# Kernel optimization log

Measured on AMD Instinct MI355X. Metric: run time of the kernel, lower is better.

The kernel has to match this reference:

```python
import jax, jax.numpy as jnp
import numpy as np
from jax import lax

B = 32768

def setup_inputs() -> dict:
    key = jax.random.key(0)
    ks = jax.random.split(key, 8)
    return {
        "x": jax.random.normal(ks[0], (B, 784), dtype=jnp.float32),
        "w_conv": jax.random.normal(ks[1], (3, 3), dtype=jnp.float32),
        "W1": jax.random.normal(ks[2], (676, 100), dtype=jnp.float32) * 0.05,
        "b1": jax.random.normal(ks[3], (100,), dtype=jnp.float32) * 0.05,
        "W2": jax.random.normal(ks[4], (100, 100), dtype=jnp.float32) * 0.05,
        "b2": jax.random.normal(ks[5], (100,), dtype=jnp.float32) * 0.05,
        "W3": jax.random.normal(ks[6], (100, 10), dtype=jnp.float32) * 0.05,
        "b3": jax.random.normal(ks[7], (10,), dtype=jnp.float32) * 0.05,
    }


def reference(x, w_conv, W1, b1, W2, b2, W3, b3):
    # x: [B, 784] -> [B, 1, 28, 28]; valid 3x3 cross-correlation (tensordot == correlation)
    xr = x.reshape(-1, 1, 28, 28)
    k = w_conv.reshape(1, 1, 3, 3)  # [out_c, in_c, kh, kw]
    conv = lax.conv_general_dilated(
        xr, k, window_strides=(1, 1), padding="VALID",
        dimension_numbers=("NCHW", "OIHW", "NCHW"))  # [B, 1, 26, 26]
    h = conv.reshape(conv.shape[0], 26 * 26)  # [B, 676]
    h = jax.nn.relu(h @ W1 + b1)
    h = jax.nn.relu(h @ W2 + b2)
    return h @ W3 + b3  # [B, 10]
```

## Files before the change

### kernel.cpp

```cpp
#include <hip/hip_runtime.h>


typedef __attribute__((ext_vector_type(8))) short bf16x8;
typedef __attribute__((ext_vector_type(4))) float f32x4;

#define KP1 832
#define NP  112
#define K2P 128
#define BM  64
#define NT  256

#define W2T_OFF (NP * KP1)
#define W3T_OFF (W2T_OFF + NP * K2P)
#define WS_USHORTS (W3T_OFF + 16 * K2P)

__device__ __forceinline__ unsigned short f2bf(float f) {
    unsigned int u = __float_as_uint(f);
    u += 0x7FFFu + ((u >> 16) & 1u);
    return (unsigned short)(u >> 16);
}

__device__ __forceinline__ unsigned int pkbf(float a, float b) {
    unsigned int r;
    asm("v_cvt_pk_bf16_f32 %0, %1, %2" : "=v"(r) : "v"(a), "v"(b));
    return r;
}

__device__ __forceinline__ bf16x8 cvt8(float4 a, float4 b) {
    union { unsigned int w[4]; bf16x8 v; } u;
    u.w[0] = pkbf(a.x, a.y);
    u.w[1] = pkbf(a.z, a.w);
    u.w[2] = pkbf(b.x, b.y);
    u.w[3] = pkbf(b.z, b.w);
    return u.v;
}

__device__ __forceinline__ void gload_lds16(const void* g, void* l) {
    __builtin_amdgcn_global_load_lds(
        (const __attribute__((address_space(1))) unsigned int*)g,
        (__attribute__((address_space(3))) unsigned int*)l, 16, 0, 0);
}

__global__ void build_weights(const float* __restrict__ w_conv,
                              const float* __restrict__ W1,
                              const float* __restrict__ W2,
                              const float* __restrict__ W3,
                              unsigned short* __restrict__ ws) {
    const int idx = blockIdx.x * 256 + threadIdx.x;
    if (idx >= WS_USHORTS) return;
    float v = 0.f;
    if (idx < W2T_OFF) {
        const int col = idx / KP1, p = idx % KP1;
        if (col < 100 && p < 784) {
            const int y = p / 28, xx = p % 28;
#pragma unroll
            for (int ky = 0; ky < 3; ++ky) {
                const int py = y - ky;
                if (py < 0 || py >= 26) continue;
#pragma unroll
                for (int kx = 0; kx < 3; ++kx) {
                    const int px = xx - kx;
                    if (px < 0 || px >= 26) continue;
                    v += w_conv[ky * 3 + kx] * W1[(py * 26 + px) * 100 + col];
                }
            }
        }
    } else if (idx < W3T_OFF) {
        const int r = idx - W2T_OFF;
        const int col = r / K2P, k = r % K2P;
        if (col < 100 && k < 100) v = W2[k * 100 + col];
    } else {
        const int r = idx - W3T_OFF;
        const int col = r / K2P, k = r % K2P;
        if (col < 10 && k < 100) v = W3[k * 10 + col];
    }
    ws[idx] = f2bf(v);
}

__global__ __launch_bounds__(NT, 2)
void fused(const float* __restrict__ x,
           const unsigned short* __restrict__ wst,
           const float* __restrict__ b1,
           const float* __restrict__ b2,
           const float* __restrict__ b3,
           float* __restrict__ out) {
    __shared__ __attribute__((aligned(16))) float          xs[2][64][64];
    __shared__ __attribute__((aligned(16))) unsigned short bs[2][112][64];
    __shared__ __attribute__((aligned(16))) unsigned short h1[64][136];
    unsigned short (*h2)[136] = reinterpret_cast<unsigned short(*)[136]>(&xs[0][0][0]);

    const int tid  = threadIdx.x;
    const int lane = tid & 63;
    const int wv   = tid >> 6;
    const int l15  = lane & 15;
    const int lk   = lane >> 4;
    const int b0   = blockIdx.x * BM;
    const int wr   = wv * 16;

    const unsigned short* weff = wst;
    const unsigned short* w2t  = wst + W2T_OFF;
    const unsigned short* w3t  = wst + W3T_OFF;

    for (int f = lane; f < 16 * 14; f += 64) {
        const int r = wr + f / 14, c = 100 + (f % 14) * 2;
        *reinterpret_cast<unsigned int*>(&h1[r][c]) = 0u;
    }

    f32x4 acc[7];
#pragma unroll
    for (int n = 0; n < 7; ++n) acc[n] = (f32x4){0.f, 0.f, 0.f, 0.f};

    auto issue = [&](int kt, int buf) {
#pragma unroll
        for (int q = 0; q < 4; ++q) {
            const int row = wr + q * 4 + (lane >> 4);
            const int col = ((lane & 15) ^ (row & 7)) * 4;
            const float* g = x + (size_t)(b0 + row) * 784 + kt * 64 + col;
            gload_lds16(g, (void*)&xs[buf][wr + q * 4][0]);
        }
#pragma unroll
        for (int i = 0; i < 4; ++i) {
            const int j = wv + 4 * i;
            if (j < 14) {
                const int row = j * 8 + (lane >> 3);
                const int col = ((lane & 7) ^ (lane >> 3)) * 8;
                const unsigned short* g = weff + (size_t)row * KP1 + kt * 64 + col;
                gload_lds16(g, (void*)&bs[buf][j * 8][0]);
            }
        }
    };

    auto computeStage = [&](int buf) {
        const int arow = wr + l15;
        const int sA = (arow & 7) << 4;
        const int sB = (l15 & 7) << 4;
        const char* ap = (const char*)&xs[buf][arow][0];
#pragma unroll
        for (int ks = 0; ks < 2; ++ks) {
            const float4 lo = *reinterpret_cast<const float4*>(ap + ((ks * 128 + lk * 32 +  0) ^ sA));
            const float4 hi = *reinterpret_cast<const float4*>(ap + ((ks * 128 + lk * 32 + 16) ^ sA));
            const bf16x8 af = cvt8(lo, hi);
#pragma unroll
            for (int n = 0; n < 7; ++n) {
                const char* bp = (const char*)&bs[buf][n * 16 + l15][0];
                const bf16x8 bfr = *reinterpret_cast<const bf16x8*>(bp + ((ks * 64 + lk * 16) ^ sB));
                acc[n] = __builtin_amdgcn_mfma_f32_16x16x32_bf16(af, bfr, acc[n], 0, 0, 0);
            }
        }
    };

    issue(0, 0);
    __syncthreads();
#pragma unroll 1
    for (int t = 0; t < 12; ++t) {
        if (t < 11) issue(t + 1, (t + 1) & 1);
        __builtin_amdgcn_sched_barrier(0);
        computeStage(t & 1);
        __syncthreads();
    }

    {
        float4 t0 = (float4){0.f, 0.f, 0.f, 0.f}, t1 = t0;
        if (lk < 2) {
            const float* xp = x + (size_t)(b0 + wr + l15) * 784 + 768 + lk * 8;
            t0 = *reinterpret_cast<const float4*>(xp);
            t1 = *reinterpret_cast<const float4*>(xp + 4);
        }
        const bf16x8 aft = cvt8(t0, t1);
#pragma unroll
        for (int n = 0; n < 7; ++n) {
            const bf16x8 bft = *reinterpret_cast<const bf16x8*>(
                weff + (size_t)(n * 16 + l15) * KP1 + 768 + lk * 8);
            acc[n] = __builtin_amdgcn_mfma_f32_16x16x32_bf16(aft, bft, acc[n], 0, 0, 0);
        }
    }

    float bias[7];
#pragma unroll
    for (int n = 0; n < 7; ++n) {
        const int c = n * 16 + l15;
        bias[n] = (c < 100) ? b1[c] : 0.f;
    }
#pragma unroll
    for (int n = 0; n < 7; ++n) {
        const int col = n * 16 + l15;
        if (col < 100)
#pragma unroll
            for (int q = 0; q < 4; ++q) {
                const float v = fmaxf(acc[n][q] + bias[n], 0.f);
                h1[wr + lk * 4 + q][col] = f2bf(v);
            }
    }
    for (int f = lane; f < 16 * 14; f += 64) {
        const int r = wr + f / 14, c = 100 + (f % 14) * 2;
        *reinterpret_cast<unsigned int*>(&h2[r][c]) = 0u;
    }
    __builtin_amdgcn_sched_barrier(0);

    f32x4 acc2[7];
#pragma unroll
    for (int n = 0; n < 7; ++n) acc2[n] = (f32x4){0.f, 0.f, 0.f, 0.f};
#pragma unroll
    for (int ks = 0; ks < 4; ++ks) {
        const int kb = ks * 32 + lk * 8;
        const bf16x8 af = *reinterpret_cast<const bf16x8*>(&h1[wr + l15][kb]);
#pragma unroll
        for (int n = 0; n < 7; ++n) {
            const bf16x8 bfr = *reinterpret_cast<const bf16x8*>(
                w2t + (size_t)(n * 16 + l15) * K2P + kb);
            acc2[n] = __builtin_amdgcn_mfma_f32_16x16x32_bf16(af, bfr, acc2[n], 0, 0, 0);
        }
    }

#pragma unroll
    for (int n = 0; n < 7; ++n) {
        const int c = n * 16 + l15;
        bias[n] = (c < 100) ? b2[c] : 0.f;
    }
#pragma unroll
    for (int n = 0; n < 7; ++n) {
        const int col = n * 16 + l15;
        if (col < 100)
#pragma unroll
            for (int q = 0; q < 4; ++q) {
                const float v = fmaxf(acc2[n][q] + bias[n], 0.f);
                h2[wr + lk * 4 + q][col] = f2bf(v);
            }
    }
    __builtin_amdgcn_sched_barrier(0);

    f32x4 acc3 = (f32x4){0.f, 0.f, 0.f, 0.f};
#pragma unroll
    for (int ks = 0; ks < 4; ++ks) {
        const int kb = ks * 32 + lk * 8;
        const bf16x8 bfr = *reinterpret_cast<const bf16x8*>(
            w3t + (size_t)l15 * K2P + kb);
        const bf16x8 af = *reinterpret_cast<const bf16x8*>(&h2[wr + l15][kb]);
        acc3 = __builtin_amdgcn_mfma_f32_16x16x32_bf16(af, bfr, acc3, 0, 0, 0);
    }

    if (l15 < 10) {
        const float bb = b3[l15];
#pragma unroll
        for (int q = 0; q < 4; ++q) {
            const int row = b0 + wr + lk * 4 + q;
            out[(size_t)row * 10 + l15] = acc3[q] + bb;
        }
    }
}

extern "C" void kernel_launch(void* const* d_in, const int* in_sizes, int n_in,
                              void* d_out, int out_size, void* d_ws, size_t ws_size,
                              hipStream_t stream) {
    const float* x      = (const float*)d_in[0];
    const float* w_conv = (const float*)d_in[1];
    const float* W1     = (const float*)d_in[2];
    const float* b1     = (const float*)d_in[3];
    const float* W2     = (const float*)d_in[4];
    const float* b2     = (const float*)d_in[5];
    const float* W3     = (const float*)d_in[6];
    const float* b3     = (const float*)d_in[7];
    float* out = (float*)d_out;
    unsigned short* ws = (unsigned short*)d_ws;

    build_weights<<<(WS_USHORTS + 255) / 256, 256, 0, stream>>>(w_conv, W1, W2, W3, ws);
    fused<<<32768 / BM, NT, 0, stream>>>(x, ws, b1, b2, b3, out);
}
```

Before: 38.35 us.

## Switch first GEMM to triple-buffered 32-wide K tiles with vmcnt waits

The first-layer GEMM loop moves from double-buffered 64-wide K tiles to triple-buffered 32-wide tiles. Waits now use explicit s_waitcnt vmcnt(4) plus a raw barrier, so two loads stay in flight while the current stage computes. The weight buffer is padded to 128 rows so each wave loads a uniform share. The aim is more overlap of global-to-LDS loads with MFMA work. In exchange there are twice as many barriers, and the hand-set vmcnt counts must match the number of outstanding loads exactly.

```diff
diff --git a/kernel.cpp b/kernel.cpp
--- a/kernel.cpp
+++ b/kernel.cpp
@@ -6,13 +6,18 @@
 
 #define KP1 832
 #define NP  112
+#define NPB 128
 #define K2P 128
 #define BM  64
 #define NT  256
 
-#define W2T_OFF (NP * KP1)
+#define W2T_OFF (NPB * KP1)
 #define W3T_OFF (W2T_OFF + NP * K2P)
 #define WS_USHORTS (W3T_OFF + 16 * K2P)
+
+#define WAITV4 asm volatile("s_waitcnt vmcnt(4)" ::: "memory")
+#define WAITV0 asm volatile("s_waitcnt vmcnt(0)" ::: "memory")
+#define BAR    __builtin_amdgcn_s_barrier()
 
 __device__ __forceinline__ unsigned short f2bf(float f) {
     unsigned int u = __float_as_uint(f);
@@ -84,8 +89,8 @@
            const float* __restrict__ b2,
            const float* __restrict__ b3,
            float* __restrict__ out) {
-    __shared__ __attribute__((aligned(16))) float          xs[2][64][64];
-    __shared__ __attribute__((aligned(16))) unsigned short bs[2][112][64];
+    __shared__ __attribute__((aligned(16))) float          xs[3][64][32];
+    __shared__ __attribute__((aligned(16))) unsigned short bs[3][128][32];
     __shared__ __attribute__((aligned(16))) unsigned short h1[64][136];
     unsigned short (*h2)[136] = reinterpret_cast<unsigned short(*)[136]>(&xs[0][0][0]);
 
@@ -110,54 +115,59 @@
 #pragma unroll
     for (int n = 0; n < 7; ++n) acc[n] = (f32x4){0.f, 0.f, 0.f, 0.f};
 
-    auto issue = [&](int kt, int buf) {
-#pragma unroll
-        for (int q = 0; q < 4; ++q) {
-            const int row = wr + q * 4 + (lane >> 4);
-            const int col = ((lane & 15) ^ (row & 7)) * 4;
-            const float* g = x + (size_t)(b0 + row) * 784 + kt * 64 + col;
-            gload_lds16(g, (void*)&xs[buf][wr + q * 4][0]);
-        }
-#pragma unroll
-        for (int i = 0; i < 4; ++i) {
-            const int j = wv + 4 * i;
-            if (j < 14) {
-                const int row = j * 8 + (lane >> 3);
-                const int col = ((lane & 7) ^ (lane >> 3)) * 8;
-                const unsigned short* g = weff + (size_t)row * KP1 + kt * 64 + col;
-                gload_lds16(g, (void*)&bs[buf][j * 8][0]);
-            }
+    const int xrow_l = lane >> 3;
+    const int xcol_b = (((lane & 7) ^ xrow_l) * 16);
+    const int brow_l = lane >> 2;
+    const int bcol_b = (((lane & 3) ^ (brow_l & 3)) * 16);
+
+    auto issue = [&](int kt, float* xb, unsigned short* bb) {
+#pragma unroll
+        for (int q = 0; q < 2; ++q) {
+            const int r = wr + 8 * q + xrow_l;
+            const char* g = (const char*)(x + (size_t)(b0 + r) * 784 + kt * 32) + xcol_b;
+            gload_lds16(g, (void*)(xb + (size_t)(wr + 8 * q) * 32));
+        }
+#pragma unroll
+        for (int q = 0; q < 2; ++q) {
+            const int r = wv * 32 + 16 * q + brow_l;
+            const char* g = (const char*)(weff + (size_t)r * KP1 + kt * 32) + bcol_b;
+            gload_lds16(g, (void*)(bb + (size_t)(wv * 32 + 16 * q) * 32));
         }
     };
 
-    auto computeStage = [&](int buf) {
-        const int arow = wr + l15;
-        const int sA = (arow & 7) << 4;
-        const int sB = (l15 & 7) << 4;
-        const char* ap = (const char*)&xs[buf][arow][0];
-#pragma unroll
-        for (int ks = 0; ks < 2; ++ks) {
-            const float4 lo = *reinterpret_cast<const float4*>(ap + ((ks * 128 + lk * 32 +  0) ^ sA));
-            const float4 hi = *reinterpret_cast<const float4*>(ap + ((ks * 128 + lk * 32 + 16) ^ sA));
-            const bf16x8 af = cvt8(lo, hi);
-#pragma unroll
-            for (int n = 0; n < 7; ++n) {
-                const char* bp = (const char*)&bs[buf][n * 16 + l15][0];
-                const bf16x8 bfr = *reinterpret_cast<const bf16x8*>(bp + ((ks * 64 + lk * 16) ^ sB));
-                acc[n] = __builtin_amdgcn_mfma_f32_16x16x32_bf16(af, bfr, acc[n], 0, 0, 0);
-            }
+    auto computeStage = [&](const float* xb, const unsigned short* bb) {
+        const int r = wr + l15;
+        const char* ap = (const char*)(xb + (size_t)r * 32);
+        const int sA = (r & 7) << 4;
+        const float4 lo = *reinterpret_cast<const float4*>(ap + ((lk * 32) ^ sA));
+        const float4 hi = *reinterpret_cast<const float4*>(ap + ((lk * 32 + 16) ^ sA));
+        const bf16x8 af = cvt8(lo, hi);
+#pragma unroll
+        for (int n = 0; n < 7; ++n) {
+            const int rn = n * 16 + l15;
+            const char* bp = (const char*)(bb + (size_t)rn * 32);
+            const bf16x8 bfr = *reinterpret_cast<const bf16x8*>(bp + ((lk * 16) ^ ((rn & 3) << 4)));
+            acc[n] = __builtin_amdgcn_mfma_f32_16x16x32_bf16(af, bfr, acc[n], 0, 0, 0);
         }
     };
 
-    issue(0, 0);
-    __syncthreads();
+    float* X0 = &xs[0][0][0]; unsigned short* B0 = &bs[0][0][0];
+    float* X1 = &xs[1][0][0]; unsigned short* B1 = &bs[1][0][0];
+    float* X2 = &xs[2][0][0]; unsigned short* B2 = &bs[2][0][0];
+
+    issue(0, X0, B0);
+    issue(1, X1, B1);
+    WAITV4; BAR;
 #pragma unroll 1
-    for (int t = 0; t < 12; ++t) {
-        if (t < 11) issue(t + 1, (t + 1) & 1);
-        __builtin_amdgcn_sched_barrier(0);
-        computeStage(t & 1);
-        __syncthreads();
-    }
+    for (int tt = 0; tt < 7; ++tt) {
+        const int t = tt * 3;
+        issue(t + 2, X2, B2); computeStage(X0, B0); WAITV4; BAR;
+        issue(t + 3, X0, B0); computeStage(X1, B1); WAITV4; BAR;
+        issue(t + 4, X1, B1); computeStage(X2, B2); WAITV4; BAR;
+    }
+    issue(23, X2, B2); computeStage(X0, B0); WAITV4; BAR;
+    computeStage(X1, B1); WAITV0; BAR;
+    computeStage(X2, B2);
 
     {
         float4 t0 = (float4){0.f, 0.f, 0.f, 0.f}, t1 = t0;
@@ -174,6 +184,7 @@
             acc[n] = __builtin_amdgcn_mfma_f32_16x16x32_bf16(aft, bft, acc[n], 0, 0, 0);
         }
     }
+    __syncthreads();
 
     float bias[7];
 #pragma unroll
```

Measured after the change: 40.13 us. 1.05x slower.

## Triple-buffer x tiles with vmcnt waits, alias h1/h2 into x buffers, vectorize weight build

Applied to the files above, without the earlier changes.

The fused kernel now keeps three x staging buffers and prefetches x two k-steps ahead. Instead of a full __syncthreads it waits with explicit s_waitcnt vmcnt counts plus s_barrier, and the main loop is fully unrolled. h1 and h2 are placed inside the x staging area, so the extra buffer adds less LDS than it would otherwise. The weight-build kernel now computes four output columns per thread using float4 loads of W1. The aim is to hide global load latency more deeply, at the cost of depending on hand-counted vmcnt values being correct.

```diff
diff --git a/kernel.cpp b/kernel.cpp
--- a/kernel.cpp
+++ b/kernel.cpp
@@ -13,6 +13,11 @@
 #define W2T_OFF (NP * KP1)
 #define W3T_OFF (W2T_OFF + NP * K2P)
 #define WS_USHORTS (W3T_OFF + 16 * K2P)
+
+#define WAITV4 asm volatile("s_waitcnt vmcnt(4)" ::: "memory")
+#define WAITV0 asm volatile("s_waitcnt vmcnt(0)" ::: "memory")
+#define BAR    __builtin_amdgcn_s_barrier()
+#define SBAR0  __builtin_amdgcn_sched_barrier(0)
 
 __device__ __forceinline__ unsigned short f2bf(float f) {
     unsigned int u = __float_as_uint(f);
@@ -47,11 +52,12 @@
                               const float* __restrict__ W3,
                               unsigned short* __restrict__ ws) {
     const int idx = blockIdx.x * 256 + threadIdx.x;
-    if (idx >= WS_USHORTS) return;
-    float v = 0.f;
-    if (idx < W2T_OFF) {
-        const int col = idx / KP1, p = idx % KP1;
-        if (col < 100 && p < 784) {
+    const int WEFF_T = 28 * KP1;
+    if (idx < WEFF_T) {
+        const int j4 = idx / KP1, p = idx % KP1;
+        const int j = j4 * 4;
+        float a0 = 0.f, a1 = 0.f, a2 = 0.f, a3 = 0.f;
+        if (p < 784 && j4 < 25) {
             const int y = p / 28, xx = p % 28;
 #pragma unroll
             for (int ky = 0; ky < 3; ++ky) {
@@ -61,20 +67,29 @@
                 for (int kx = 0; kx < 3; ++kx) {
                     const int px = xx - kx;
                     if (px < 0 || px >= 26) continue;
-                    v += w_conv[ky * 3 + kx] * W1[(py * 26 + px) * 100 + col];
+                    const float wc = w_conv[ky * 3 + kx];
+                    const float4 w = *reinterpret_cast<const float4*>(
+                        W1 + (size_t)(py * 26 + px) * 100 + j);
+                    a0 = fmaf(wc, w.x, a0); a1 = fmaf(wc, w.y, a1);
+                    a2 = fmaf(wc, w.z, a2); a3 = fmaf(wc, w.w, a3);
                 }
             }
         }
-    } else if (idx < W3T_OFF) {
-        const int r = idx - W2T_OFF;
+        ws[(size_t)(j + 0) * KP1 + p] = f2bf(a0);
+        ws[(size_t)(j + 1) * KP1 + p] = f2bf(a1);
+        ws[(size_t)(j + 2) * KP1 + p] = f2bf(a2);
+        ws[(size_t)(j + 3) * KP1 + p] = f2bf(a3);
+    } else if (idx < WEFF_T + NP * K2P) {
+        const int r = idx - WEFF_T;
         const int col = r / K2P, k = r % K2P;
-        if (col < 100 && k < 100) v = W2[k * 100 + col];
-    } else {
-        const int r = idx - W3T_OFF;
+        float v = (col < 100 && k < 100) ? W2[k * 100 + col] : 0.f;
+        ws[W2T_OFF + r] = f2bf(v);
+    } else if (idx < WEFF_T + NP * K2P + 16 * K2P) {
+        const int r = idx - WEFF_T - NP * K2P;
         const int col = r / K2P, k = r % K2P;
-        if (col < 10 && k < 100) v = W3[k * 10 + col];
-    }
-    ws[idx] = f2bf(v);
+        float v = (col < 10 && k < 100) ? W3[k * 10 + col] : 0.f;
+        ws[W3T_OFF + r] = f2bf(v);
+    }
 }
 
 __global__ __launch_bounds__(NT, 2)
@@ -84,10 +99,11 @@
            const float* __restrict__ b2,
            const float* __restrict__ b3,
            float* __restrict__ out) {
-    __shared__ __attribute__((aligned(16))) float          xs[2][64][64];
+    __shared__ __attribute__((aligned(16))) float          xs[3][64][64];
     __shared__ __attribute__((aligned(16))) unsigned short bs[2][112][64];
-    __shared__ __attribute__((aligned(16))) unsigned short h1[64][136];
-    unsigned short (*h2)[136] = reinterpret_cast<unsigned short(*)[136]>(&xs[0][0][0]);
+    unsigned short (*h1)[136] = reinterpret_cast<unsigned short(*)[136]>(&xs[0][0][0]);
+    unsigned short (*h2)[136] = reinterpret_cast<unsigned short(*)[136]>(
+        (char*)&xs[0][0][0] + 17408);
 
     const int tid  = threadIdx.x;
     const int lane = tid & 63;
@@ -101,62 +117,70 @@
     const unsigned short* w2t  = wst + W2T_OFF;
     const unsigned short* w3t  = wst + W3T_OFF;
 
-    for (int f = lane; f < 16 * 14; f += 64) {
-        const int r = wr + f / 14, c = 100 + (f % 14) * 2;
-        *reinterpret_cast<unsigned int*>(&h1[r][c]) = 0u;
-    }
-
     f32x4 acc[7];
 #pragma unroll
     for (int n = 0; n < 7; ++n) acc[n] = (f32x4){0.f, 0.f, 0.f, 0.f};
 
-    auto issue = [&](int kt, int buf) {
+    auto issueX = [&](int kt, float* xb) {
 #pragma unroll
         for (int q = 0; q < 4; ++q) {
-            const int row = wr + q * 4 + (lane >> 4);
-            const int col = ((lane & 15) ^ (row & 7)) * 4;
-            const float* g = x + (size_t)(b0 + row) * 784 + kt * 64 + col;
-            gload_lds16(g, (void*)&xs[buf][wr + q * 4][0]);
-        }
-#pragma unroll
-        for (int i = 0; i < 4; ++i) {
-            const int j = wv + 4 * i;
-            if (j < 14) {
-                const int row = j * 8 + (lane >> 3);
-                const int col = ((lane & 7) ^ (lane >> 3)) * 8;
-                const unsigned short* g = weff + (size_t)row * KP1 + kt * 64 + col;
-                gload_lds16(g, (void*)&bs[buf][j * 8][0]);
-            }
+            const int rowbase = wr + 4 * q;
+            const int r = rowbase + (lane >> 4);
+            const int chunk = (lane & 15) ^ (r & 7);
+            const char* g = (const char*)(x + (size_t)(b0 + r) * 784 + kt * 64)
+                          + chunk * 16;
+            gload_lds16(g, (char*)xb + rowbase * 256);
         }
     };
-
-    auto computeStage = [&](int buf) {
-        const int arow = wr + l15;
-        const int sA = (arow & 7) << 4;
-        const int sB = (l15 & 7) << 4;
-        const char* ap = (const char*)&xs[buf][arow][0];
+    auto issueB = [&](int kt, unsigned short* bb) {
+#pragma unroll
+        for (int k = 0; k < 4; ++k) {
+            const int i = wv + 4 * k;
+            if (i < 14) {
+                const int rowbase = 8 * i;
+                const int r = rowbase + (lane >> 3);
+                const int chunk = (lane & 7) ^ (r & 7);
+                const char* g = (const char*)(weff + (size_t)r * KP1 + kt * 64)
+                              + chunk * 16;
+                gload_lds16(g, (char*)bb + rowbase * 128);
+            }
+        }
+    };
+
+    auto computeStage = [&](const float* xb, const unsigned short* bb) {
+        const int r = wr + l15;
+        const int sA = (r & 7) << 4;
+        const char* ap = (const char*)xb + r * 256;
 #pragma unroll
         for (int ks = 0; ks < 2; ++ks) {
-            const float4 lo = *reinterpret_cast<const float4*>(ap + ((ks * 128 + lk * 32 +  0) ^ sA));
-            const float4 hi = *reinterpret_cast<const float4*>(ap + ((ks * 128 + lk * 32 + 16) ^ sA));
+            const int base = ks * 128 + lk * 32;
+            const float4 lo = *reinterpret_cast<const float4*>(ap + ((base     ) ^ sA));
+            const float4 hi = *reinterpret_cast<const float4*>(ap + ((base + 16) ^ sA));
             const bf16x8 af = cvt8(lo, hi);
 #pragma unroll
             for (int n = 0; n < 7; ++n) {
-                const char* bp = (const char*)&bs[buf][n * 16 + l15][0];
-                const bf16x8 bfr = *reinterpret_cast<const bf16x8*>(bp + ((ks * 64 + lk * 16) ^ sB));
+                const int rn = n * 16 + l15;
+                const char* bp = (const char*)bb + rn * 128;
+                const bf16x8 bfr = *reinterpret_cast<const bf16x8*>(
+                    bp + ((ks * 64 + lk * 16) ^ ((rn & 7) << 4)));
                 acc[n] = __builtin_amdgcn_mfma_f32_16x16x32_bf16(af, bfr, acc[n], 0, 0, 0);
             }
         }
     };
 
-    issue(0, 0);
-    __syncthreads();
-#pragma unroll 1
+    float*          X[3] = {&xs[0][0][0], &xs[1][0][0], &xs[2][0][0]};
+    unsigned short* Bf[2] = {&bs[0][0][0], &bs[1][0][0]};
+
+    issueX(0, X[0]); issueB(0, Bf[0]); issueX(1, X[1]);
+    WAITV4; BAR;
+#pragma unroll
     for (int t = 0; t < 12; ++t) {
-        if (t < 11) issue(t + 1, (t + 1) & 1);
-        __builtin_amdgcn_sched_barrier(0);
-        computeStage(t & 1);
-        __syncthreads();
+        if (t < 11) issueB(t + 1, Bf[(t + 1) & 1]);
+        if (t < 10) issueX(t + 2, X[(t + 2) % 3]);
+        SBAR0;
+        computeStage(X[t % 3], Bf[t & 1]);
+        if (t < 10)      { WAITV4; BAR; }
+        else if (t == 10){ WAITV0; BAR; }
     }
 
     {
@@ -174,6 +198,7 @@
             acc[n] = __builtin_amdgcn_mfma_f32_16x16x32_bf16(aft, bft, acc[n], 0, 0, 0);
         }
     }
+    __syncthreads();
 
     float bias[7];
 #pragma unroll
@@ -193,9 +218,10 @@
     }
     for (int f = lane; f < 16 * 14; f += 64) {
         const int r = wr + f / 14, c = 100 + (f % 14) * 2;
+        *reinterpret_cast<unsigned int*>(&h1[r][c]) = 0u;
         *reinterpret_cast<unsigned int*>(&h2[r][c]) = 0u;
     }
-    __builtin_amdgcn_sched_barrier(0);
+    SBAR0;
 
     f32x4 acc2[7];
 #pragma unroll
@@ -227,7 +253,7 @@
                 h2[wr + lk * 4 + q][col] = f2bf(v);
             }
     }
-    __builtin_amdgcn_sched_barrier(0);
+    SBAR0;
 
     f32x4 acc3 = (f32x4){0.f, 0.f, 0.f, 0.f};
 #pragma unroll
@@ -263,6 +289,7 @@
     float* out = (float*)d_out;
     unsigned short* ws = (unsigned short*)d_ws;
 
-    build_weights<<<(WS_USHORTS + 255) / 256, 256, 0, stream>>>(w_conv, W1, W2, W3, ws);
+    const int total = 28 * KP1 + NP * K2P + 16 * K2P;
+    build_weights<<<(total + 255) / 256, 256, 0, stream>>>(w_conv, W1, W2, W3, ws);
     fused<<<32768 / BM, NT, 0, stream>>>(x, ws, b1, b2, b3, out);
 }
```

After: 36.47 us. 1.05x faster.
